# Optimization experiments

Measured on AMD Instinct MI355X. Metric: run time of the kernel, lower is better.

The kernel has to match this reference:

```python
import jax, jax.numpy as jnp
import numpy as np

D_NUM = 24
N_FREQ = 16
D_EMB = 32
D_IN_RAW = 32
D_IN_ENC = D_NUM * D_EMB + (D_IN_RAW - D_NUM)  # 776
DIM = 512
D_OUT = 10
TEMP = 1.0
EPS = 1e-07


def setup_inputs() -> dict:
    key = jax.random.key(0)
    ks = jax.random.split(key, 8)
    x = jax.random.normal(ks[0], (1024, D_IN_RAW), dtype=jnp.float32)
    candidate_x = jax.random.normal(ks[1], (100000, D_IN_RAW), dtype=jnp.float32)
    candidate_y = jax.random.randint(ks[2], (100000,), 0, D_OUT)
    # PLR embedding params
    frequencies = 0.01 * jax.random.normal(ks[3], (D_NUM, N_FREQ), dtype=jnp.float32)
    plr_w = jax.random.normal(ks[4], (D_EMB, 2 * N_FREQ), dtype=jnp.float32) / np.sqrt(2 * N_FREQ)
    plr_b = jnp.zeros((D_EMB,), dtype=jnp.float32)
    # encoder Linear(776 -> 512)
    enc_w = jax.random.normal(ks[5], (DIM, D_IN_ENC), dtype=jnp.float32) / np.sqrt(D_IN_ENC)
    enc_b = jnp.zeros((DIM,), dtype=jnp.float32)
    return {"x": x, "candidate_x": candidate_x, "candidate_y": candidate_y,
            "frequencies": frequencies, "plr_w": plr_w, "plr_b": plr_b,
            "enc_w": enc_w, "enc_b": enc_b, "is_train": 0}


def _encode(v, frequencies, plr_w, plr_b, enc_w, enc_b):
    # v: [B, 32]; split numeric / categorical
    v_num, v_cat = v[:, :D_NUM], v[:, D_NUM:]
    # PeriodicEmbeddings: [B, d_num, n_freq]
    z = 2.0 * jnp.pi * frequencies[None] * v_num[..., None]
    z = jnp.concatenate([jnp.cos(z), jnp.sin(z)], axis=-1)  # [B, d_num, 2*n_freq]
    z = jax.nn.relu(jnp.einsum('bnf,ef->bne', z, plr_w) + plr_b)  # [B, d_num, d_emb]
    z = z.reshape(v.shape[0], -1)  # [B, d_num*d_emb]
    feat = jnp.concatenate([z, v_cat], axis=-1)  # [B, 776]
    return feat @ enc_w.T + enc_b  # [B, dim]


def reference(x, candidate_x, candidate_y, frequencies, plr_w, plr_b, enc_w, enc_b, is_train):
    # eval path: is_train == 0, y is None
    xe = _encode(x, frequencies, plr_w, plr_b, enc_w, enc_b)            # [N, dim]
    ce = _encode(candidate_x, frequencies, plr_w, plr_b, enc_w, enc_b)  # [M, dim]
    # Euclidean cdist via ||a||^2 + ||b||^2 - 2 a.b
    sq = (jnp.sum(xe * xe, -1)[:, None] + jnp.sum(ce * ce, -1)[None, :]
          - 2.0 * (xe @ ce.T))
    dist = jnp.sqrt(jnp.maximum(sq, 1e-12)) / TEMP  # [N, M]
    probs = jax.nn.softmax(-dist, axis=-1)
    onehot = jax.nn.one_hot(candidate_y, D_OUT, dtype=xe.dtype)  # [M, d_out]
    logits = probs @ onehot  # [N, d_out]
    return jnp.log(logits + EPS)
```

## Files before the change

kernel.cpp:

```cpp
#include <hip/hip_runtime.h>


#define TWO_PI 6.283185307179586f
#define N_CAND 100000
#define N_CPAD 100224
#define N_CB   (N_CPAD / 64)
#define N_Q    1024
#define KENC   832

typedef unsigned short ushort_t;
typedef unsigned int uint_t;
typedef __attribute__((ext_vector_type(8))) short short8;
typedef __attribute__((ext_vector_type(4))) float f32x4;

__device__ __forceinline__ float bf2f(ushort_t h) {
    union { uint_t u; float f; } c; c.u = ((uint_t)h) << 16; return c.f;
}
__device__ __forceinline__ ushort_t f2bf(float f) {
    union { float f; uint_t u; } c; c.f = f;
    uint_t u = c.u + 0x7fffu + ((c.u >> 16) & 1u);
    return (ushort_t)(u >> 16);
}

__device__ __forceinline__ void glds16(const void* g, void* l) {
    __builtin_amdgcn_global_load_lds(
        (const __attribute__((address_space(1))) void*)g,
        (__attribute__((address_space(3))) void*)l, 16, 0, 0);
}

__global__ __launch_bounds__(256) void wsplit_kernel(
    const float* __restrict__ encw, ushort_t* __restrict__ w_hi)
{
    int idx = blockIdx.x * 256 + threadIdx.x;
    if (idx >= 512 * KENC) return;
    int n = idx / KENC, k = idx - n * KENC;
    float w = (k < 776) ? encw[n * 776 + k] : 0.f;
    w_hi[idx] = f2bf(w);
}

__global__ __launch_bounds__(256) void hist_kernel(
    const int* __restrict__ cy, int* __restrict__ hist,
    int* __restrict__ perm, int* __restrict__ scls)
{
    __shared__ int lh[10];
    int t = threadIdx.x;
    long j = (long)blockIdx.x * 256 + t;
    if (t < 10) lh[t] = 0;
    __syncthreads();
    if (j < N_CAND) atomicAdd(&lh[cy[j]], 1);
    __syncthreads();
    if (t < 10 && lh[t] > 0) atomicAdd(&hist[t], lh[t]);
    if (blockIdx.x == 0 && t < N_CPAD - N_CAND) {
        perm[N_CAND + t] = 0;
        scls[N_CAND + t] = 0;
    }
}

__global__ void prefix_kernel(const int* __restrict__ hist, int* __restrict__ cursor)
{
    if (threadIdx.x == 0) {
        int run = 0;
        for (int c = 0; c < 10; ++c) { cursor[c] = run; run += hist[c]; }
    }
}

__global__ __launch_bounds__(256) void scatter_kernel(
    const int* __restrict__ cy, int* __restrict__ cursor,
    int* __restrict__ perm, int* __restrict__ scls)
{
    __shared__ int lh[10], lbase[10];
    int t = threadIdx.x;
    long j = (long)blockIdx.x * 256 + t;
    if (t < 10) lh[t] = 0;
    __syncthreads();
    int cls = -1;
    if (j < N_CAND) { cls = cy[j]; atomicAdd(&lh[cls], 1); }
    __syncthreads();
    if (t < 10 && lh[t] > 0) lbase[t] = atomicAdd(&cursor[t], lh[t]);
    __syncthreads();
    if (j < N_CAND) {
        int pos = atomicAdd(&lbase[cls], 1);
        perm[pos] = (int)j;
        scls[pos] = cls;
    }
}

__global__ __launch_bounds__(256) void plr_kernel(
    const float* __restrict__ vin,
    int nsrc, long src_base,
    const int*   __restrict__ perm,
    const float* __restrict__ freq,
    const float* __restrict__ plrw,
    const float* __restrict__ plrb,
    ushort_t*    __restrict__ feat_out)
{
    __shared__ float s_cx[32 * 32];
    __shared__ float s_freq[24 * 16];
    __shared__ __align__(16) ushort_t s_feat[32 * KENC];

    const int t = threadIdx.x;
    const long lbase = (long)blockIdx.x * 32;
    const long gbase = src_base + lbase;
    const int lane = t & 63, w = t >> 6;
    const int lr = lane & 15, g = lane >> 4;

    {
        long idx = gbase + (t >> 3);
        long row;
        if (perm) row = perm[idx];
        else      row = (idx > (long)nsrc - 1) ? nsrc - 1 : idx;
        ((float4*)s_cx)[t] = ((const float4*)(vin + row * 32))[t & 7];
    }
    if (t < 96) {
        float4 f = ((const float4*)freq)[t];
        f.x *= TWO_PI; f.y *= TWO_PI; f.z *= TWO_PI; f.w *= TWO_PI;
        ((float4*)s_freq)[t] = f;
    }
    for (int i = t; i < 896; i += 256) {
        int row = i / 28, o = (i - row * 28) * 2;
        *(uint_t*)&s_feat[row * KENC + 776 + o] = 0u;
    }

    short8 pbh[2], pbl[2];
    float pbias[2];
    #pragma unroll
    for (int n = 0; n < 2; ++n) {
        int e = n * 16 + lr;
        const float* pr = plrw + e * 32 + g * 8;
        float wv[8];
        *(float4*)&wv[0] = *(const float4*)pr;
        *(float4*)&wv[4] = *(const float4*)(pr + 4);
        #pragma unroll
        for (int j = 0; j < 8; ++j) {
            ushort_t h = f2bf(wv[j]);
            pbh[n][j] = (short)h;
            pbl[n][j] = (short)f2bf(wv[j] - bf2f(h));
        }
        pbias[n] = plrb[e];
    }
    __syncthreads();

    const bool use_sin = (lane >= 32);
    const int f0 = (g & 1) * 8;
    for (int i = 0; i < 12; ++i) {
        const int tile = w * 12 + i;
        const int m_a = tile * 16 + lr;
        const int rowa = m_a / 24, na = m_a - rowa * 24;
        const float v = s_cx[rowa * 32 + na];
        float ang[8];
        *(float4*)&ang[0] = *(const float4*)&s_freq[na * 16 + f0];
        *(float4*)&ang[4] = *(const float4*)&s_freq[na * 16 + f0 + 4];
        short8 af;
        #pragma unroll
        for (int j = 0; j < 8; ++j) {
            float sv, cv;
            __sincosf(ang[j] * v, &sv, &cv);
            af[j] = (short)f2bf(use_sin ? sv : cv);
        }
        f32x4 c0 = {0.f, 0.f, 0.f, 0.f}, c1 = {0.f, 0.f, 0.f, 0.f};
        c0 = __builtin_amdgcn_mfma_f32_16x16x32_bf16(af, pbh[0], c0, 0, 0, 0);
        c0 = __builtin_amdgcn_mfma_f32_16x16x32_bf16(af, pbl[0], c0, 0, 0, 0);
        c1 = __builtin_amdgcn_mfma_f32_16x16x32_bf16(af, pbh[1], c1, 0, 0, 0);
        c1 = __builtin_amdgcn_mfma_f32_16x16x32_bf16(af, pbl[1], c1, 0, 0, 0);
        #pragma unroll
        for (int r = 0; r < 4; ++r) {
            const int m_c = tile * 16 + g * 4 + r;
            const int rowc = m_c / 24, nc = m_c - rowc * 24;
            s_feat[rowc * KENC + nc * 32 + lr]      = f2bf(fmaxf(c0[r] + pbias[0], 0.f));
            s_feat[rowc * KENC + nc * 32 + 16 + lr] = f2bf(fmaxf(c1[r] + pbias[1], 0.f));
        }
    }
    {
        int c = t >> 3, j = t & 7;
        s_feat[c * KENC + 768 + j] = f2bf(s_cx[c * 32 + 24 + j]);
    }
    __syncthreads();

    uint4* dst = (uint4*)(feat_out + lbase * KENC);
    const uint4* src = (const uint4*)s_feat;
    #pragma unroll
    for (int i = 0; i < 13; ++i)
        dst[t + 256 * i] = src[t + 256 * i];
}

__global__ __launch_bounds__(256) void enc_gemm_kernel(
    const ushort_t* __restrict__ feat,
    int nrb,
    long mbase,
    const ushort_t* __restrict__ w_hi,
    const float* __restrict__ encb,
    ushort_t* __restrict__ enc_out,
    float*    __restrict__ sq_out)
{
    __shared__ __align__(16) ushort_t s_A[128 * 64];
    __shared__ __align__(16) ushort_t s_B[128 * 64];
    __shared__ float s_sq[128];

    const int id = blockIdx.x;
    const int rb = (id >> 5) * 8 + (id & 7);
    if (rb >= nrb) return;
    const int nbase = ((id >> 3) & 3) * 128;
    const long mloc = (long)rb * 128;

    const int t = threadIdx.x;
    const int lane = t & 63, w = t >> 6;
    const int lr = lane & 15, g = lane >> 4;
    const int mrow = (w & 1) * 64, ncol = (w >> 1) * 64;
    const int wu = t & ~63;
    const int xr = lr & 7;

    if (t < 128) s_sq[t] = 0.f;

    const ushort_t* fsrc[4];
    const ushort_t* wsrc[4];
    char* ldsA[4]; char* ldsB[4];
    #pragma unroll
    for (int s = 0; s < 4; ++s) {
        int idx = t + 256 * s;
        int row = idx >> 3;
        int seg = ((idx & 7) ^ (row & 7)) * 8;
        fsrc[s] = &feat[(mloc + row) * KENC + seg];
        wsrc[s] = &w_hi[(size_t)(nbase + row) * KENC + seg];
        ldsA[s] = (char*)s_A + (size_t)(wu + 256 * s) * 16;
        ldsB[s] = (char*)s_B + (size_t)(wu + 256 * s) * 16;
    }

    f32x4 zero4 = {0.f, 0.f, 0.f, 0.f};
    f32x4 acc[4][4];
    #pragma unroll
    for (int mt = 0; mt < 4; ++mt)
        #pragma unroll
        for (int nt = 0; nt < 4; ++nt) acc[mt][nt] = zero4;

    for (int kc = 0; kc < 13; ++kc) {
        const int k0 = kc * 64;
        __syncthreads();
        #pragma unroll
        for (int s = 0; s < 4; ++s) {
            glds16(fsrc[s] + k0, ldsA[s]);
            glds16(wsrc[s] + k0, ldsB[s]);
        }
        __syncthreads();
        #pragma unroll
        for (int kk = 0; kk < 2; ++kk) {
            const int pos = ((kk * 4 + g) ^ xr) * 8;
            short8 a[4], b[4];
            #pragma unroll
            for (int mt = 0; mt < 4; ++mt)
                a[mt] = *(const short8*)&s_A[(mrow + mt * 16 + lr) * 64 + pos];
            #pragma unroll
            for (int nt = 0; nt < 4; ++nt)
                b[nt] = *(const short8*)&s_B[(ncol + nt * 16 + lr) * 64 + pos];
            #pragma unroll
            for (int mt = 0; mt < 4; ++mt)
                #pragma unroll
                for (int nt = 0; nt < 4; ++nt)
                    acc[mt][nt] = __builtin_amdgcn_mfma_f32_16x16x32_bf16(
                        a[mt], b[nt], acc[mt][nt], 0, 0, 0);
        }
    }

    float bias[4];
    #pragma unroll
    for (int nt = 0; nt < 4; ++nt) bias[nt] = encb[nbase + ncol + nt * 16 + lr];

    #pragma unroll
    for (int mt = 0; mt < 4; ++mt) {
        float sqr[4] = {0.f, 0.f, 0.f, 0.f};
        #pragma unroll
        for (int nt = 0; nt < 4; ++nt) {
            #pragma unroll
            for (int r = 0; r < 4; ++r) {
                float v = acc[mt][nt][r] + bias[nt];
                ushort_t hb = f2bf(v);
                float vb = bf2f(hb);
                sqr[r] += vb * vb;
                enc_out[(mbase + mloc + mrow + mt * 16 + g * 4 + r) * 512
                        + nbase + ncol + nt * 16 + lr] = hb;
            }
        }
        #pragma unroll
        for (int r = 0; r < 4; ++r) {
            float vs = sqr[r];
            vs += __shfl_xor(vs, 1);
            vs += __shfl_xor(vs, 2);
            vs += __shfl_xor(vs, 4);
            vs += __shfl_xor(vs, 8);
            if (lr == 0) atomicAdd(&s_sq[mrow + mt * 16 + g * 4 + r], vs);
        }
    }
    __syncthreads();
    if (t < 128) atomicAdd(&sq_out[mbase + mloc + t], s_sq[t]);
}

__global__ __launch_bounds__(256, 3) void dist_kernel(
    const ushort_t* __restrict__ xe,
    const ushort_t* __restrict__ ce,
    const float*    __restrict__ xsq,
    const float*    __restrict__ csq,
    const int*      __restrict__ scls,
    float*          __restrict__ gbins)
{
    __shared__ __align__(16) ushort_t s_ce[64 * 128];
    __shared__ float s_csq[64];
    __shared__ int   s_y[64];

    const int id = blockIdx.x;
    const int cband = (id >> 5) * 8 + (id & 7);
    if (cband >= N_CB) return;
    const int qbase = ((id >> 3) & 3) * 256;
    const long cbase = (long)cband * 64;

    const int t = threadIdx.x;
    const int lane = t & 63, w = t >> 6;
    const int lr = lane & 15, g = lane >> 4;
    const int wu = t & ~63;

    if (t < 64) {
        long jc = cbase + t;
        s_y[t]   = scls[jc];
        s_csq[t] = (jc < N_CAND) ? csq[jc] : 1e30f;
    }

    f32x4 zero4 = {0.f, 0.f, 0.f, 0.f};
    f32x4 acc[4][4];
    #pragma unroll
    for (int mt = 0; mt < 4; ++mt)
        #pragma unroll
        for (int nt = 0; nt < 4; ++nt) acc[mt][nt] = zero4;

    for (int kc = 0; kc < 4; ++kc) {
        const int k0 = kc * 128;
        __syncthreads();
        #pragma unroll
        for (int s = 0; s < 4; ++s) {
            int idx = t + 256 * s;
            int row = idx >> 4, pos = idx & 15;
            int seg = pos ^ (row & 15);
            glds16(&ce[(cbase + row) * 512 + k0 + seg * 8],
                   (char*)s_ce + (size_t)(wu + 256 * s) * 16);
        }
        short8 a[4][4];
        #pragma unroll
        for (int kk = 0; kk < 4; ++kk)
            #pragma unroll
            for (int mt = 0; mt < 4; ++mt)
                a[kk][mt] = *(const short8*)
                    &xe[(size_t)(qbase + w * 64 + mt * 16 + lr) * 512 + k0 + kk * 32 + g * 8];
        __syncthreads();
        #pragma unroll
        for (int kk = 0; kk < 4; ++kk) {
            short8 b[4];
            #pragma unroll
            for (int nt = 0; nt < 4; ++nt) {
                int pos = (kk * 4 + g) ^ lr;
                b[nt] = *(const short8*)&s_ce[(nt * 16 + lr) * 128 + pos * 8];
            }
            #pragma unroll
            for (int mt = 0; mt < 4; ++mt)
                #pragma unroll
                for (int nt = 0; nt < 4; ++nt)
                    acc[mt][nt] = __builtin_amdgcn_mfma_f32_16x16x32_bf16(
                        a[kk][mt], b[nt], acc[mt][nt], 0, 0, 0);
        }
    }

    float xq[4][4];
    #pragma unroll
    for (int mt = 0; mt < 4; ++mt)
        #pragma unroll
        for (int r = 0; r < 4; ++r)
            xq[mt][r] = xsq[qbase + w * 64 + mt * 16 + g * 4 + r];

    float cq[4]; int ycls[4];
    #pragma unroll
    for (int nt = 0; nt < 4; ++nt) {
        cq[nt]   = s_csq[nt * 16 + lr];
        ycls[nt] = s_y[nt * 16 + lr];
    }
    #pragma unroll
    for (int mt = 0; mt < 4; ++mt)
        #pragma unroll
        for (int nt = 0; nt < 4; ++nt)
            #pragma unroll
            for (int r = 0; r < 4; ++r) {
                float sqv = xq[mt][r] + cq[nt] - 2.f * acc[mt][nt][r];
                acc[mt][nt][r] = __expf(-sqrtf(fmaxf(sqv, 1e-12f)));
            }

    long chi = cbase + 63; if (chi > N_CAND - 1) chi = N_CAND - 1;
    const int cls_lo = s_y[0];
    const int cls_hi = (chi >= cbase) ? s_y[(int)(chi - cbase)] : s_y[0];

    for (int cls = cls_lo; cls <= cls_hi; ++cls) {
        #pragma unroll
        for (int mt = 0; mt < 4; ++mt) {
            #pragma unroll
            for (int r = 0; r < 4; ++r) {
                float s = 0.f;
                #pragma unroll
                for (int nt = 0; nt < 4; ++nt)
                    s += (ycls[nt] == cls) ? acc[mt][nt][r] : 0.f;
                s += __shfl_xor(s, 1);
                s += __shfl_xor(s, 2);
                s += __shfl_xor(s, 4);
                s += __shfl_xor(s, 8);
                if (lr == 0)
                    atomicAdd(&gbins[(size_t)(qbase + w * 64 + mt * 16 + g * 4 + r) * 10 + cls], s);
            }
        }
    }
}

__global__ __launch_bounds__(256) void final_kernel(
    const float* __restrict__ gbins, float* __restrict__ out)
{
    int q = blockIdx.x * 256 + threadIdx.x;
    if (q >= N_Q) return;
    float b[10], Z = 0.f;
    #pragma unroll
    for (int c = 0; c < 10; ++c) { b[c] = gbins[q * 10 + c]; Z += b[c]; }
    float inv = 1.f / Z;
    #pragma unroll
    for (int c = 0; c < 10; ++c)
        out[q * 10 + c] = logf(b[c] * inv + 1e-7f);
}

extern "C" void kernel_launch(void* const* d_in, const int* in_sizes, int n_in,
                              void* d_out, int out_size, void* d_ws, size_t ws_size,
                              hipStream_t stream) {
    const float* x  = (const float*)d_in[0];
    const float* cx = (const float*)d_in[1];
    const int*   cy = (const int*)d_in[2];
    const float* fr = (const float*)d_in[3];
    const float* pw = (const float*)d_in[4];
    const float* pb = (const float*)d_in[5];
    const float* ew = (const float*)d_in[6];
    const float* eb = (const float*)d_in[7];
    float* out = (float*)d_out;

    char* ws = (char*)d_ws;
    ushort_t* ce   = (ushort_t*)(ws);
    ushort_t* xe   = (ushort_t*)(ws + 102629376);
    float*    csq  = (float*)   (ws + 103677952);
    float*    xsq  = (float*)   (ws + 104078848);
    float*    gbin = (float*)   (ws + 104082944);
    int*      hist = (int*)     (ws + 104123904);
    int*      curs = (int*)     (ws + 104123968);
    ushort_t* w_hi = (ushort_t*)(ws + 104124032);
    ushort_t* fq   = (ushort_t*)(ws + 105827968);
    int*      perm = (int*)     (ws + 107531904);
    int*      scls = (int*)     (ws + 107932800);
    ushort_t* fc   = (ushort_t*)(ws + 108333696);

    long avail = (long)ws_size - 108333696L;
    long slab = avail / (KENC * 2);
    slab &= ~127L;
    if (slab > N_CPAD) slab = N_CPAD;
    if (slab < 128)    slab = 128;

    hipMemsetAsync(csq, 0, 446016, stream);
    wsplit_kernel<<<1664, 256, 0, stream>>>(ew, w_hi);

    hist_kernel<<<391, 256, 0, stream>>>(cy, hist, perm, scls);
    prefix_kernel<<<1, 64, 0, stream>>>(hist, curs);
    scatter_kernel<<<391, 256, 0, stream>>>(cy, curs, perm, scls);

    plr_kernel<<<N_Q / 32, 256, 0, stream>>>(x, N_Q, 0, nullptr, fr, pw, pb, fq);
    enc_gemm_kernel<<<32, 256, 0, stream>>>(fq, 8, 0, w_hi, eb, xe, xsq);

    for (long sb = 0; sb < N_CPAD; sb += slab) {
        long rows = (N_CPAD - sb < slab) ? (N_CPAD - sb) : slab;
        int nrb = (int)(rows / 128);
        plr_kernel<<<rows / 32, 256, 0, stream>>>(cx, N_CAND, sb, perm, fr, pw, pb, fc);
        enc_gemm_kernel<<<((nrb + 7) / 8) * 32, 256, 0, stream>>>(
            fc, nrb, sb, w_hi, eb, ce, csq);
    }

    int ngroups = (N_CB + 7) / 8;
    dist_kernel<<<ngroups * 32, 256, 0, stream>>>(xe, ce, xsq, csq, scls, gbin);
    final_kernel<<<4, 256, 0, stream>>>(gbin, out);
}
```

Measured before the change: 545.4 us.

## Fuse PLR embedding into encoder GEMM, computing A tiles on the fly

The PLR periodic embedding is now computed inside the encoder GEMM: each k-chunk of the A operand is produced directly into swizzled LDS with sincos and MFMA, so the bf16 feature matrix is never written to or read back from global memory. The separate plr kernel, the feature workspace slabs and the slab loop are removed. The cost is that each of the four column blocks that share a row block recomputes the PLR features, roughly quadrupling the sincos work, and the GEMM loop now has serial compute between the weight loads and the MFMAs.

Measured after the change: 596.2 us. 1.09x slower.

```diff
diff --git a/kernel.cpp b/kernel.cpp
--- a/kernel.cpp
+++ b/kernel.cpp
@@ -5,6 +5,7 @@
 #define N_CAND 100000
 #define N_CPAD 100224
 #define N_CB   (N_CPAD / 64)
+#define N_RB   (N_CPAD / 128)
 #define N_Q    1024
 #define KENC   832
 
@@ -85,40 +86,52 @@
     }
 }
 
-__global__ __launch_bounds__(256) void plr_kernel(
+__global__ __launch_bounds__(256) void enc_fused_kernel(
     const float* __restrict__ vin,
-    int nsrc, long src_base,
+    int nsrc, int nrb,
     const int*   __restrict__ perm,
     const float* __restrict__ freq,
     const float* __restrict__ plrw,
     const float* __restrict__ plrb,
-    ushort_t*    __restrict__ feat_out)
-{
-    __shared__ float s_cx[32 * 32];
+    const ushort_t* __restrict__ w_hi,
+    const float* __restrict__ encb,
+    ushort_t* __restrict__ enc_out,
+    float*    __restrict__ sq_out)
+{
+    __shared__ __align__(16) ushort_t s_A[128 * 64];
+    __shared__ __align__(16) ushort_t s_B[128 * 64];
+    __shared__ float s_cx[128 * 32];
     __shared__ float s_freq[24 * 16];
-    __shared__ __align__(16) ushort_t s_feat[32 * KENC];
+    __shared__ float s_sq[128];
+
+    const int id = blockIdx.x;
+    const int rb = (id >> 5) * 8 + (id & 7);
+    if (rb >= nrb) return;
+    const int nbase = ((id >> 3) & 3) * 128;
+    const long mloc = (long)rb * 128;
 
     const int t = threadIdx.x;
-    const long lbase = (long)blockIdx.x * 32;
-    const long gbase = src_base + lbase;
     const int lane = t & 63, w = t >> 6;
     const int lr = lane & 15, g = lane >> 4;
-
-    {
-        long idx = gbase + (t >> 3);
+    const int mrow = (w & 1) * 64, ncol = (w >> 1) * 64;
+    const int wu = t & ~63;
+    const int xr = lr & 7;
+
+    if (t < 128) s_sq[t] = 0.f;
+
+    #pragma unroll
+    for (int i = 0; i < 4; ++i) {
+        int idx = t + 256 * i;
+        long src_i = mloc + (idx >> 3);
         long row;
-        if (perm) row = perm[idx];
-        else      row = (idx > (long)nsrc - 1) ? nsrc - 1 : idx;
-        ((float4*)s_cx)[t] = ((const float4*)(vin + row * 32))[t & 7];
+        if (perm) row = perm[src_i];
+        else      row = (src_i > (long)nsrc - 1) ? nsrc - 1 : src_i;
+        ((float4*)s_cx)[idx] = ((const float4*)(vin + row * 32))[idx & 7];
     }
     if (t < 96) {
         float4 f = ((const float4*)freq)[t];
         f.x *= TWO_PI; f.y *= TWO_PI; f.z *= TWO_PI; f.w *= TWO_PI;
         ((float4*)s_freq)[t] = f;
-    }
-    for (int i = t; i < 896; i += 256) {
-        int row = i / 28, o = (i - row * 28) * 2;
-        *(uint_t*)&s_feat[row * KENC + 776 + o] = 0u;
     }
 
     short8 pbh[2], pbl[2];
@@ -138,90 +151,15 @@
         }
         pbias[n] = plrb[e];
     }
-    __syncthreads();
-
-    const bool use_sin = (lane >= 32);
-    const int f0 = (g & 1) * 8;
-    for (int i = 0; i < 12; ++i) {
-        const int tile = w * 12 + i;
-        const int m_a = tile * 16 + lr;
-        const int rowa = m_a / 24, na = m_a - rowa * 24;
-        const float v = s_cx[rowa * 32 + na];
-        float ang[8];
-        *(float4*)&ang[0] = *(const float4*)&s_freq[na * 16 + f0];
-        *(float4*)&ang[4] = *(const float4*)&s_freq[na * 16 + f0 + 4];
-        short8 af;
-        #pragma unroll
-        for (int j = 0; j < 8; ++j) {
-            float sv, cv;
-            __sincosf(ang[j] * v, &sv, &cv);
-            af[j] = (short)f2bf(use_sin ? sv : cv);
-        }
-        f32x4 c0 = {0.f, 0.f, 0.f, 0.f}, c1 = {0.f, 0.f, 0.f, 0.f};
-        c0 = __builtin_amdgcn_mfma_f32_16x16x32_bf16(af, pbh[0], c0, 0, 0, 0);
-        c0 = __builtin_amdgcn_mfma_f32_16x16x32_bf16(af, pbl[0], c0, 0, 0, 0);
-        c1 = __builtin_amdgcn_mfma_f32_16x16x32_bf16(af, pbh[1], c1, 0, 0, 0);
-        c1 = __builtin_amdgcn_mfma_f32_16x16x32_bf16(af, pbl[1], c1, 0, 0, 0);
-        #pragma unroll
-        for (int r = 0; r < 4; ++r) {
-            const int m_c = tile * 16 + g * 4 + r;
-            const int rowc = m_c / 24, nc = m_c - rowc * 24;
-            s_feat[rowc * KENC + nc * 32 + lr]      = f2bf(fmaxf(c0[r] + pbias[0], 0.f));
-            s_feat[rowc * KENC + nc * 32 + 16 + lr] = f2bf(fmaxf(c1[r] + pbias[1], 0.f));
-        }
-    }
-    {
-        int c = t >> 3, j = t & 7;
-        s_feat[c * KENC + 768 + j] = f2bf(s_cx[c * 32 + 24 + j]);
-    }
-    __syncthreads();
-
-    uint4* dst = (uint4*)(feat_out + lbase * KENC);
-    const uint4* src = (const uint4*)s_feat;
-    #pragma unroll
-    for (int i = 0; i < 13; ++i)
-        dst[t + 256 * i] = src[t + 256 * i];
-}
-
-__global__ __launch_bounds__(256) void enc_gemm_kernel(
-    const ushort_t* __restrict__ feat,
-    int nrb,
-    long mbase,
-    const ushort_t* __restrict__ w_hi,
-    const float* __restrict__ encb,
-    ushort_t* __restrict__ enc_out,
-    float*    __restrict__ sq_out)
-{
-    __shared__ __align__(16) ushort_t s_A[128 * 64];
-    __shared__ __align__(16) ushort_t s_B[128 * 64];
-    __shared__ float s_sq[128];
-
-    const int id = blockIdx.x;
-    const int rb = (id >> 5) * 8 + (id & 7);
-    if (rb >= nrb) return;
-    const int nbase = ((id >> 3) & 3) * 128;
-    const long mloc = (long)rb * 128;
-
-    const int t = threadIdx.x;
-    const int lane = t & 63, w = t >> 6;
-    const int lr = lane & 15, g = lane >> 4;
-    const int mrow = (w & 1) * 64, ncol = (w >> 1) * 64;
-    const int wu = t & ~63;
-    const int xr = lr & 7;
-
-    if (t < 128) s_sq[t] = 0.f;
-
-    const ushort_t* fsrc[4];
+
     const ushort_t* wsrc[4];
-    char* ldsA[4]; char* ldsB[4];
+    char* ldsB[4];
     #pragma unroll
     for (int s = 0; s < 4; ++s) {
         int idx = t + 256 * s;
         int row = idx >> 3;
         int seg = ((idx & 7) ^ (row & 7)) * 8;
-        fsrc[s] = &feat[(mloc + row) * KENC + seg];
         wsrc[s] = &w_hi[(size_t)(nbase + row) * KENC + seg];
-        ldsA[s] = (char*)s_A + (size_t)(wu + 256 * s) * 16;
         ldsB[s] = (char*)s_B + (size_t)(wu + 256 * s) * 16;
     }
 
@@ -231,14 +169,67 @@
     for (int mt = 0; mt < 4; ++mt)
         #pragma unroll
         for (int nt = 0; nt < 4; ++nt) acc[mt][nt] = zero4;
+
+    const bool use_sin = (lane >= 32);
+    const int f0 = (g & 1) * 8;
+
+    __syncthreads();
 
     for (int kc = 0; kc < 13; ++kc) {
         const int k0 = kc * 64;
         __syncthreads();
         #pragma unroll
-        for (int s = 0; s < 4; ++s) {
-            glds16(fsrc[s] + k0, ldsA[s]);
+        for (int s = 0; s < 4; ++s)
             glds16(wsrc[s] + k0, ldsB[s]);
+
+        if (kc < 12) {
+            #pragma unroll
+            for (int i = 0; i < 4; ++i) {
+                const int tile = w * 4 + i;
+                const int m_a = tile * 16 + lr;
+                const int rowa = m_a >> 1;
+                const int na = 2 * kc + (m_a & 1);
+                const float v = s_cx[rowa * 32 + na];
+                float ang[8];
+                *(float4*)&ang[0] = *(const float4*)&s_freq[na * 16 + f0];
+                *(float4*)&ang[4] = *(const float4*)&s_freq[na * 16 + f0 + 4];
+                short8 af;
+                #pragma unroll
+                for (int j = 0; j < 8; ++j) {
+                    float sv, cv;
+                    __sincosf(ang[j] * v, &sv, &cv);
+                    af[j] = (short)f2bf(use_sin ? sv : cv);
+                }
+                f32x4 c0 = {0.f, 0.f, 0.f, 0.f}, c1 = {0.f, 0.f, 0.f, 0.f};
+                c0 = __builtin_amdgcn_mfma_f32_16x16x32_bf16(af, pbh[0], c0, 0, 0, 0);
+                c0 = __builtin_amdgcn_mfma_f32_16x16x32_bf16(af, pbl[0], c0, 0, 0, 0);
+                c1 = __builtin_amdgcn_mfma_f32_16x16x32_bf16(af, pbh[1], c1, 0, 0, 0);
+                c1 = __builtin_amdgcn_mfma_f32_16x16x32_bf16(af, pbl[1], c1, 0, 0, 0);
+                #pragma unroll
+                for (int r = 0; r < 4; ++r) {
+                    const int m_c = tile * 16 + g * 4 + r;
+                    const int rowc = m_c >> 1, npc = m_c & 1;
+                    const int kc0 = npc * 32 + lr;
+                    const int kc1 = kc0 + 16;
+                    s_A[rowc * 64 + (((kc0 >> 3) ^ (rowc & 7)) << 3) + (kc0 & 7)]
+                        = f2bf(fmaxf(c0[r] + pbias[0], 0.f));
+                    s_A[rowc * 64 + (((kc1 >> 3) ^ (rowc & 7)) << 3) + (kc1 & 7)]
+                        = f2bf(fmaxf(c1[r] + pbias[1], 0.f));
+                }
+            }
+        } else {
+            uint4 z = {0u, 0u, 0u, 0u};
+            #pragma unroll
+            for (int i = 0; i < 4; ++i)
+                ((uint4*)s_A)[t + 256 * i] = z;
+            __syncthreads();
+            {
+                int row = t >> 1, j0 = (t & 1) * 4;
+                int ad = row * 64 + ((row & 7) << 3) + j0;
+                #pragma unroll
+                for (int j = 0; j < 4; ++j)
+                    s_A[ad + j] = f2bf(s_cx[row * 32 + 24 + j0 + j]);
+            }
         }
         __syncthreads();
         #pragma unroll
@@ -275,7 +266,7 @@
                 ushort_t hb = f2bf(v);
                 float vb = bf2f(hb);
                 sqr[r] += vb * vb;
-                enc_out[(mbase + mloc + mrow + mt * 16 + g * 4 + r) * 512
+                enc_out[(mloc + mrow + mt * 16 + g * 4 + r) * 512
                         + nbase + ncol + nt * 16 + lr] = hb;
             }
         }
@@ -290,7 +281,7 @@
         }
     }
     __syncthreads();
-    if (t < 128) atomicAdd(&sq_out[mbase + mloc + t], s_sq[t]);
+    if (t < 128) atomicAdd(&sq_out[mloc + t], s_sq[t]);
 }
 
 __global__ __launch_bounds__(256, 3) void dist_kernel(
@@ -448,16 +439,8 @@
     int*      hist = (int*)     (ws + 104123904);
     int*      curs = (int*)     (ws + 104123968);
     ushort_t* w_hi = (ushort_t*)(ws + 104124032);
-    ushort_t* fq   = (ushort_t*)(ws + 105827968);
-    int*      perm = (int*)     (ws + 107531904);
-    int*      scls = (int*)     (ws + 107932800);
-    ushort_t* fc   = (ushort_t*)(ws + 108333696);
-
-    long avail = (long)ws_size - 108333696L;
-    long slab = avail / (KENC * 2);
-    slab &= ~127L;
-    if (slab > N_CPAD) slab = N_CPAD;
-    if (slab < 128)    slab = 128;
+    int*      perm = (int*)     (ws + 104976000);
+    int*      scls = (int*)     (ws + 105376896);
 
     hipMemsetAsync(csq, 0, 446016, stream);
     wsplit_kernel<<<1664, 256, 0, stream>>>(ew, w_hi);
@@ -466,18 +449,13 @@
     prefix_kernel<<<1, 64, 0, stream>>>(hist, curs);
     scatter_kernel<<<391, 256, 0, stream>>>(cy, curs, perm, scls);
 
-    plr_kernel<<<N_Q / 32, 256, 0, stream>>>(x, N_Q, 0, nullptr, fr, pw, pb, fq);
-    enc_gemm_kernel<<<32, 256, 0, stream>>>(fq, 8, 0, w_hi, eb, xe, xsq);
-
-    for (long sb = 0; sb < N_CPAD; sb += slab) {
-        long rows = (N_CPAD - sb < slab) ? (N_CPAD - sb) : slab;
-        int nrb = (int)(rows / 128);
-        plr_kernel<<<rows / 32, 256, 0, stream>>>(cx, N_CAND, sb, perm, fr, pw, pb, fc);
-        enc_gemm_kernel<<<((nrb + 7) / 8) * 32, 256, 0, stream>>>(
-            fc, nrb, sb, w_hi, eb, ce, csq);
-    }
-
-    int ngroups = (N_CB + 7) / 8;
-    dist_kernel<<<ngroups * 32, 256, 0, stream>>>(xe, ce, xsq, csq, scls, gbin);
+    enc_fused_kernel<<<32, 256, 0, stream>>>(
+        x, N_Q, 8, nullptr, fr, pw, pb, w_hi, eb, xe, xsq);
+
+    enc_fused_kernel<<<((N_RB + 7) / 8) * 32, 256, 0, stream>>>(
+        cx, N_CAND, N_RB, perm, fr, pw, pb, w_hi, eb, ce, csq);
+
+    dist_kernel<<<((N_CB + 7) / 8) * 32, 256, 0, stream>>>(
+        xe, ce, xsq, csq, scls, gbin);
     final_kernel<<<4, 256, 0, stream>>>(gbin, out);
 }
```
